# Performance work log

Measured on AMD Instinct MI355X. Metric: run time of the kernel, lower is better.

## Reference

```python
import jax, jax.numpy as jnp
import numpy as np
import math

B, S, DIM, H = 2, 2048, 1024, 16
Q_DIM = 64                 # cfg.pair_dim
V_DIM = Q_DIM * 3 // 2     # 96
MAX_POS = 2048             # cfg.rope_max_position
EPS = 1e-8
SOFTCAP = 5.0


def apply_rope(x):
    # x: [B, S, H, D]; faithful to torch version: freq = 1/logspace(0, log10(max_pos), D//2)
    D = x.shape[-1]
    nf = D // 2
    freq = 1.0 / jnp.logspace(0.0, math.log10(MAX_POS), nf, dtype=x.dtype)   # [nf]
    positions = jnp.arange(x.shape[1], dtype=x.dtype)                         # [S]
    theta = positions[:, None] * freq                                         # [S, nf]
    sin_t = jnp.sin(theta)[None, :, None, :]                                  # [1,S,1,nf]
    cos_t = jnp.cos(theta)[None, :, None, :]
    x1 = x[..., ::2]
    x2 = x[..., 1::2]
    return jnp.concatenate([x1 * cos_t - x2 * sin_t, x1 * sin_t + x2 * cos_t], axis=-1)


def setup_inputs() -> dict:
    key = jax.random.key(0)
    ks = jax.random.split(key, 9)
    x = jax.random.normal(ks[0], (B, S, DIM), dtype=jnp.float32)
    attention_bias = jax.random.normal(ks[1], (B, H, S, S), dtype=jnp.float32)
    rms_weight = jnp.ones((DIM,), dtype=jnp.float32)
    sd = 1.0 / math.sqrt(DIM)
    Wq = jax.random.normal(ks[2], (DIM, H * Q_DIM), dtype=jnp.float32) * sd
    Wk = jax.random.normal(ks[3], (DIM, Q_DIM), dtype=jnp.float32) * sd
    Wv = jax.random.normal(ks[4], (DIM, V_DIM), dtype=jnp.float32) * sd
    bv = jax.random.normal(ks[5], (V_DIM,), dtype=jnp.float32) * sd
    Wo = jax.random.normal(ks[6], (H * V_DIM, DIM), dtype=jnp.float32) / math.sqrt(H * V_DIM)
    bo = jax.random.normal(ks[7], (DIM,), dtype=jnp.float32) * sd
    return {"x": x, "attention_bias": attention_bias, "rms_weight": rms_weight,
            "Wq": Wq, "Wk": Wk, "Wv": Wv, "bv": bv, "Wo": Wo, "bo": bo}


def reference(x, attention_bias, rms_weight, Wq, Wk, Wv, bv, Wo, bo):
    # RMSNorm
    xn = x * rms_weight / jnp.sqrt(jnp.mean(x * x, axis=-1, keepdims=True) + EPS)
    # projections (MQA: single shared k and v head)
    q = (xn @ Wq).reshape(B, S, H, Q_DIM)          # [B,S,H,Dq]
    k = xn @ Wk                                     # [B,S,Dq]
    v = xn @ Wv + bv                                # [B,S,Dv]
    # RoPE
    q = apply_rope(q)
    k = apply_rope(k[:, :, None, :])[:, :, 0, :]
    # attention logits with tanh soft-cap and external bias: [B,H,S,S]
    logits = jnp.einsum('bihd,bjd->bhij', q, k)
    logits = jnp.tanh((logits + attention_bias) / SOFTCAP) * SOFTCAP
    attn = jax.nn.softmax(logits, axis=-1)
    # context: shared V across heads
    ctx = jnp.einsum('bhij,bjd->bihd', attn, v).reshape(B, S, H * V_DIM)
    return ctx @ Wo + bo
```

## Files before the change

kernel.cpp:

```cpp
#include <hip/hip_runtime.h>
#include <math.h>

#define B_   2
#define S_   2048
#define DIM_ 1024
#define H_   16
#define QD_  64
#define VD_  96
#define NQKV 1184
#define EPS_ 1e-8f

using half_t = _Float16;
using half8  = __attribute__((ext_vector_type(8))) _Float16;
using half4v = __attribute__((ext_vector_type(4))) _Float16;
using f32x4  = __attribute__((ext_vector_type(4))) float;

__global__ __launch_bounds__(256) void rmsnorm_h(const float* __restrict__ x,
                                                 const float* __restrict__ w,
                                                 half_t* __restrict__ xn) {
    int row = blockIdx.x;
    int t = threadIdx.x;
    float4 v = ((const float4*)(x + (size_t)row * DIM_))[t];
    float ss = v.x * v.x + v.y * v.y + v.z * v.z + v.w * v.w;
#pragma unroll
    for (int off = 32; off > 0; off >>= 1) ss += __shfl_down(ss, off, 64);
    __shared__ float wsum[4];
    if ((t & 63) == 0) wsum[t >> 6] = ss;
    __syncthreads();
    float tot = wsum[0] + wsum[1] + wsum[2] + wsum[3];
    float scale = rsqrtf(tot * (1.0f / DIM_) + EPS_);
    float4 wv = ((const float4*)w)[t];
    half4v o;
    o[0] = (half_t)(v.x * wv.x * scale);
    o[1] = (half_t)(v.y * wv.y * scale);
    o[2] = (half_t)(v.z * wv.z * scale);
    o[3] = (half_t)(v.w * wv.w * scale);
    ((half4v*)(xn + (size_t)row * DIM_))[t] = o;
}

template <typename TIN>
__global__ __launch_bounds__(256) void transpose_cvt(const TIN* __restrict__ in,
                                                     half_t* __restrict__ out,
                                                     int R, int C, int ldin,
                                                     size_t zin, size_t zout) {
    __shared__ float tile[32][33];
    in += (size_t)blockIdx.z * zin;
    out += (size_t)blockIdx.z * zout;
    int tx = threadIdx.x & 31, ty = threadIdx.x >> 5;
#pragma unroll
    for (int i = 0; i < 32; i += 8) {
        int r = blockIdx.y * 32 + ty + i, c = blockIdx.x * 32 + tx;
        tile[ty + i][tx] = (float)in[(size_t)r * ldin + c];
    }
    __syncthreads();
#pragma unroll
    for (int i = 0; i < 32; i += 8) {
        int orow = blockIdx.x * 32 + ty + i, ocol = blockIdx.y * 32 + tx;
        out[(size_t)orow * R + ocol] = (half_t)tile[tx][ty + i];
    }
}

__global__ __launch_bounds__(256) void fill_qkv_bias(const float* __restrict__ bv,
                                                     float* __restrict__ bq) {
    int i = blockIdx.x * 256 + threadIdx.x;
    if (i < NQKV) bq[i] = (i >= H_ * QD_ + QD_) ? bv[i - (H_ * QD_ + QD_)] : 0.0f;
}

template <typename OutT, bool BIAS>
__global__ __launch_bounds__(256) void gemm_h(const half_t* __restrict__ A,
                                              const half_t* __restrict__ BT,
                                              OutT* __restrict__ C,
                                              const float* __restrict__ bias,
                                              int M, int N, int K) {
    __shared__ half_t As[64][40];
    __shared__ half_t Bs[128][40];
    int t = threadIdx.x;
    int w = t >> 6, lane = t & 63, l15 = lane & 15, l4 = lane >> 4;
    int wm = (w >> 1) * 32, wn = (w & 1) * 64;
    int m0 = blockIdx.y * 64, n0 = blockIdx.x * 128;
    int r0 = t >> 2, off0 = (t & 3) * 8;
    f32x4 acc[2][4] = {};
    const half8 hz = {};

    const half_t* Ap = A + (size_t)(m0 + r0) * K + off0;
    const half_t* Bp0 = BT + (size_t)(n0 + r0) * K + off0;
    const half_t* Bp1 = Bp0 + (size_t)64 * K;
    bool bok0 = (n0 + r0) < N, bok1 = (n0 + r0 + 64) < N;

    half8 a0 = *(const half8*)Ap;
    half8 b0 = bok0 ? *(const half8*)Bp0 : hz;
    half8 b1 = bok1 ? *(const half8*)Bp1 : hz;

    for (int k0 = 0; k0 < K; k0 += 32) {
        __syncthreads();
        *(half8*)&As[r0][off0] = a0;
        *(half8*)&Bs[r0][off0] = b0;
        *(half8*)&Bs[r0 + 64][off0] = b1;
        __syncthreads();
        if (k0 + 32 < K) {
            a0 = *(const half8*)(Ap + k0 + 32);
            b0 = bok0 ? *(const half8*)(Bp0 + k0 + 32) : hz;
            b1 = bok1 ? *(const half8*)(Bp1 + k0 + 32) : hz;
        }
        half8 af[2], bf[4];
#pragma unroll
        for (int mt = 0; mt < 2; ++mt) af[mt] = *(const half8*)&As[wm + mt * 16 + l15][l4 * 8];
#pragma unroll
        for (int nt = 0; nt < 4; ++nt) bf[nt] = *(const half8*)&Bs[wn + nt * 16 + l15][l4 * 8];
#pragma unroll
        for (int mt = 0; mt < 2; ++mt)
#pragma unroll
            for (int nt = 0; nt < 4; ++nt)
                acc[mt][nt] =
                    __builtin_amdgcn_mfma_f32_16x16x32_f16(af[mt], bf[nt], acc[mt][nt], 0, 0, 0);
    }

#pragma unroll
    for (int mt = 0; mt < 2; ++mt)
#pragma unroll
        for (int nt = 0; nt < 4; ++nt) {
            int n = n0 + wn + nt * 16 + l15;
            if (n < N) {
#pragma unroll
                for (int reg = 0; reg < 4; ++reg) {
                    int m = m0 + wm + mt * 16 + l4 * 4 + reg;
                    float v = acc[mt][nt][reg];
                    if (BIAS) v += bias[n];
                    C[(size_t)m * N + n] = (OutT)v;
                }
            }
        }
}

__global__ __launch_bounds__(256) void rope_h(const half_t* __restrict__ in, int ldin,
                                              half_t* __restrict__ out,
                                              int hc, int total_pairs) {
    int p = blockIdx.x * 256 + threadIdx.x;
    if (p >= total_pairs) return;
    int i = p & 31;
    int chunk = p >> 5;
    int row = chunk / hc;
    int h = chunk - row * hc;
    int s = row & (S_ - 1);
    const half_t* src = in + (size_t)row * ldin + h * 64 + 2 * i;
    float x1 = (float)src[0], x2 = (float)src[1];
    float freq = exp2f((float)i * (-11.0f / 31.0f));
    float th = (float)s * freq;
    float sn, cs;
    sincosf(th, &sn, &cs);
    half_t* dst = out + (size_t)chunk * 64;
    dst[i] = (half_t)(x1 * cs - x2 * sn);
    dst[i + 32] = (half_t)(x1 * sn + x2 * cs);
}

#define C1_ 0.57707801635558534f
#define C2_ 14.426950408889634f

__global__ __launch_bounds__(256, 4) void attn_mfma(const half_t* __restrict__ qh,
                                                    const half_t* __restrict__ kh,
                                                    const half_t* __restrict__ vt,
                                                    const float* __restrict__ bias,
                                                    half_t* __restrict__ ctx) {
    __shared__ half_t ks[64][72];
    __shared__ half_t vs[96][72];
    __shared__ half_t ps[4][16][72];

    int t = threadIdx.x;
    int w = t >> 6, lane = t & 63, l15 = lane & 15, l4 = lane >> 4;
    int i0 = blockIdx.x * 64, h = blockIdx.y, b = blockIdx.z;

    const half_t* qbase =
        qh + (((size_t)(b * S_ + i0 + w * 16 + l15) * H_ + h) << 6) + l4 * 8;
    half8 qf0 = *(const half8*)qbase;
    half8 qf1 = *(const half8*)(qbase + 32);

    f32x4 cacc[6] = {};
    float rsum = 0.f;

    int sr = t >> 3, so = (t & 7) * 8;
    const float* bbase =
        bias + ((size_t)(b * H_ + h) * S_ + i0 + w * 16 + l15) * S_ + l4 * 4;
    const half_t* krow0 = kh + (((size_t)b * S_ + sr) << 6) + so;
    const half_t* krow1 = krow0 + ((size_t)32 << 6);
    const half_t* vrow0 = vt + ((size_t)b * 96 + sr) * S_ + so;
    const half_t* vrow1 = vrow0 + (size_t)32 * S_;
    const half_t* vrow2 = vrow0 + (size_t)64 * S_;

    half8 kr0, kr1, vr0, vr1, vr2;
    f32x4 bc[4], bn[4];

    kr0 = *(const half8*)krow0;
    kr1 = *(const half8*)krow1;
    vr0 = *(const half8*)vrow0;
    vr1 = *(const half8*)vrow1;
    vr2 = *(const half8*)vrow2;
#pragma unroll
    for (int nt = 0; nt < 4; ++nt) {
        f32x4 bb = __builtin_nontemporal_load((const f32x4*)(bbase + nt * 16));
#pragma unroll
        for (int e = 0; e < 4; ++e) bc[nt][e] = bb[e] * C1_;
    }

    *(half8*)&ks[sr][so] = kr0;
    *(half8*)&ks[sr + 32][so] = kr1;
    *(half8*)&vs[sr][so] = vr0;
    *(half8*)&vs[sr + 32][so] = vr1;
    *(half8*)&vs[sr + 64][so] = vr2;
    __syncthreads();

    for (int j0 = 0; j0 < S_; j0 += 64) {
        int jn = j0 + 64;
        bool more = jn < S_;

        if (more) {
            kr0 = *(const half8*)(krow0 + ((size_t)jn << 6));
            kr1 = *(const half8*)(krow1 + ((size_t)jn << 6));
            vr0 = *(const half8*)(vrow0 + jn);
            vr1 = *(const half8*)(vrow1 + jn);
            vr2 = *(const half8*)(vrow2 + jn);
#pragma unroll
            for (int nt = 0; nt < 4; ++nt)
                bn[nt] = __builtin_nontemporal_load((const f32x4*)(bbase + jn + nt * 16));
        }

#pragma unroll
        for (int nt = 0; nt < 4; ++nt) {
            f32x4 s = {};
            half8 kb0 = *(const half8*)&ks[nt * 16 + l15][l4 * 8];
            half8 kb1 = *(const half8*)&ks[nt * 16 + l15][32 + l4 * 8];
            __builtin_amdgcn_s_setprio(1);
            s = __builtin_amdgcn_mfma_f32_16x16x32_f16(kb0, qf0, s, 0, 0, 0);
            s = __builtin_amdgcn_mfma_f32_16x16x32_f16(kb1, qf1, s, 0, 0, 0);
            __builtin_amdgcn_s_setprio(0);
            half4v ph;
#pragma unroll
            for (int reg = 0; reg < 4; ++reg) {
                float u = __builtin_amdgcn_exp2f(fmaf(C1_, s[reg], bc[nt][reg]));
                float p = __builtin_amdgcn_exp2f(-C2_ * __builtin_amdgcn_rcpf(u + 1.0f));
                rsum += p;
                ph[reg] = (half_t)p;
            }
            *(half4v*)&ps[w][l15][nt * 16 + l4 * 4] = ph;
        }

        __builtin_amdgcn_s_setprio(1);
#pragma unroll
        for (int hf = 0; hf < 2; ++hf) {
            half8 af = *(const half8*)&ps[w][l15][hf * 32 + l4 * 8];
#pragma unroll
            for (int nt = 0; nt < 6; ++nt) {
                half8 vv = *(const half8*)&vs[nt * 16 + l15][hf * 32 + l4 * 8];
                cacc[nt] = __builtin_amdgcn_mfma_f32_16x16x32_f16(af, vv, cacc[nt], 0, 0, 0);
            }
        }
        __builtin_amdgcn_s_setprio(0);

        if (more) {
            __syncthreads();
            *(half8*)&ks[sr][so] = kr0;
            *(half8*)&ks[sr + 32][so] = kr1;
            *(half8*)&vs[sr][so] = vr0;
            *(half8*)&vs[sr + 32][so] = vr1;
            *(half8*)&vs[sr + 64][so] = vr2;
            __syncthreads();
#pragma unroll
            for (int nt = 0; nt < 4; ++nt)
#pragma unroll
                for (int e = 0; e < 4; ++e) bc[nt][e] = bn[nt][e] * C1_;
        }
    }

    rsum += __shfl_xor(rsum, 16, 64);
    rsum += __shfl_xor(rsum, 32, 64);
    float rinv = __builtin_amdgcn_rcpf(rsum);
    float rr[4];
#pragma unroll
    for (int reg = 0; reg < 4; ++reg) rr[reg] = __shfl(rinv, l4 * 4 + reg, 64);

#pragma unroll
    for (int nt = 0; nt < 6; ++nt)
#pragma unroll
        for (int reg = 0; reg < 4; ++reg) {
            int i = i0 + w * 16 + l4 * 4 + reg;
            ctx[((size_t)(b * S_ + i) * H_ + h) * VD_ + nt * 16 + l15] =
                (half_t)(cacc[nt][reg] * rr[reg]);
        }
}

extern "C" void kernel_launch(void* const* d_in, const int* in_sizes, int n_in,
                              void* d_out, int out_size, void* d_ws, size_t ws_size,
                              hipStream_t stream) {
    (void)in_sizes; (void)n_in; (void)out_size; (void)ws_size;
    const float* x  = (const float*)d_in[0];
    const float* ab = (const float*)d_in[1];
    const float* rw = (const float*)d_in[2];
    const float* Wq = (const float*)d_in[3];
    const float* Wk = (const float*)d_in[4];
    const float* Wv = (const float*)d_in[5];
    const float* bv = (const float*)d_in[6];
    const float* Wo = (const float*)d_in[7];
    const float* bo = (const float*)d_in[8];
    float* out = (float*)d_out;

    const size_t R = (size_t)B_ * S_;
    half_t* p = (half_t*)d_ws;
    half_t* xn_h  = p;  p += R * DIM_;
    half_t* qkv_h = p;  p += R * NQKV;
    half_t* q_h   = p;  p += R * DIM_;
    half_t* k_h   = p;  p += R * QD_;
    half_t* vtb   = p;  p += R * VD_;
    half_t* ctx_h = p;  p += R * H_ * VD_;
    half_t* WqkvT = p;  p += (size_t)NQKV * DIM_;
    half_t* WoT   = p;  p += (size_t)(H_ * VD_) * DIM_;
    float*  bqkv  = (float*)p;  p += 2 * NQKV;

    rmsnorm_h<<<dim3(R), 256, 0, stream>>>(x, rw, xn_h);

    half_t* WqT = WqkvT;
    half_t* WkT = WqkvT + (size_t)(H_ * QD_) * DIM_;
    half_t* WvT = WkT + (size_t)QD_ * DIM_;
    transpose_cvt<float><<<dim3(32, 32, 1), 256, 0, stream>>>(Wq, WqT, DIM_, H_ * QD_,
                                                              H_ * QD_, 0, 0);
    transpose_cvt<float><<<dim3(2, 32, 1), 256, 0, stream>>>(Wk, WkT, DIM_, QD_, QD_, 0, 0);
    transpose_cvt<float><<<dim3(3, 32, 1), 256, 0, stream>>>(Wv, WvT, DIM_, VD_, VD_, 0, 0);
    transpose_cvt<float><<<dim3(32, 48, 1), 256, 0, stream>>>(Wo, WoT, H_ * VD_, DIM_,
                                                              DIM_, 0, 0);
    fill_qkv_bias<<<dim3((NQKV + 255) / 256), 256, 0, stream>>>(bv, bqkv);

    gemm_h<half_t, true><<<dim3(10, 64), 256, 0, stream>>>(xn_h, WqkvT, qkv_h, bqkv,
                                                           (int)R, NQKV, DIM_);

    rope_h<<<dim3((R * H_ * 32) / 256), 256, 0, stream>>>(qkv_h, NQKV, q_h, H_,
                                                          (int)(R * H_ * 32));
    rope_h<<<dim3((R * 32) / 256), 256, 0, stream>>>(qkv_h + H_ * QD_, NQKV, k_h, 1,
                                                     (int)(R * 32));

    transpose_cvt<half_t><<<dim3(3, 64, 2), 256, 0, stream>>>(
        qkv_h + H_ * QD_ + QD_, vtb, S_, VD_, NQKV, (size_t)S_ * NQKV, (size_t)VD_ * S_);

    attn_mfma<<<dim3(S_ / 64, H_, B_), 256, 0, stream>>>(q_h, k_h, vtb, ab, ctx_h);

    gemm_h<float, true><<<dim3(8, 64), 256, 0, stream>>>(ctx_h, WoT, out, bo,
                                                         (int)R, DIM_, H_ * VD_);
}
```

Before: 831.7 us.

## Load K/V MFMA fragments directly from global memory, drop shared staging and barriers

The attention kernel no longer stages K and V tiles in shared memory with two block barriers per iteration. Each wave now loads its MFMA operand fragments for K and V straight from global memory, relying on L2/L1 caching since all waves and blocks share the same K/V. The occupancy hint drops from 4 to 3 blocks per SM to leave room for the extra fragment registers. The cost is 4x redundant global/L1 traffic for K/V across waves and exposed load latency, since the loads are no longer prefetched one iteration ahead.

```diff
diff --git a/kernel.cpp b/kernel.cpp
--- a/kernel.cpp
+++ b/kernel.cpp
@@ -156,13 +156,11 @@
 #define C1_ 0.57707801635558534f
 #define C2_ 14.426950408889634f
 
-__global__ __launch_bounds__(256, 4) void attn_mfma(const half_t* __restrict__ qh,
+__global__ __launch_bounds__(256, 3) void attn_mfma(const half_t* __restrict__ qh,
                                                     const half_t* __restrict__ kh,
                                                     const half_t* __restrict__ vt,
                                                     const float* __restrict__ bias,
                                                     half_t* __restrict__ ctx) {
-    __shared__ half_t ks[64][72];
-    __shared__ half_t vs[96][72];
     __shared__ half_t ps[4][16][72];
 
     int t = threadIdx.x;
@@ -177,60 +175,47 @@
     f32x4 cacc[6] = {};
     float rsum = 0.f;
 
-    int sr = t >> 3, so = (t & 7) * 8;
     const float* bbase =
         bias + ((size_t)(b * H_ + h) * S_ + i0 + w * 16 + l15) * S_ + l4 * 4;
-    const half_t* krow0 = kh + (((size_t)b * S_ + sr) << 6) + so;
-    const half_t* krow1 = krow0 + ((size_t)32 << 6);
-    const half_t* vrow0 = vt + ((size_t)b * 96 + sr) * S_ + so;
-    const half_t* vrow1 = vrow0 + (size_t)32 * S_;
-    const half_t* vrow2 = vrow0 + (size_t)64 * S_;
-
-    half8 kr0, kr1, vr0, vr1, vr2;
+    const half_t* kfb = kh + (((size_t)b * S_ + l15) << 6) + l4 * 8;
+    const half_t* vfb = vt + ((size_t)b * 96 + l15) * S_ + l4 * 8;
+
     f32x4 bc[4], bn[4];
-
-    kr0 = *(const half8*)krow0;
-    kr1 = *(const half8*)krow1;
-    vr0 = *(const half8*)vrow0;
-    vr1 = *(const half8*)vrow1;
-    vr2 = *(const half8*)vrow2;
 #pragma unroll
     for (int nt = 0; nt < 4; ++nt) {
         f32x4 bb = __builtin_nontemporal_load((const f32x4*)(bbase + nt * 16));
 #pragma unroll
         for (int e = 0; e < 4; ++e) bc[nt][e] = bb[e] * C1_;
     }
-
-    *(half8*)&ks[sr][so] = kr0;
-    *(half8*)&ks[sr + 32][so] = kr1;
-    *(half8*)&vs[sr][so] = vr0;
-    *(half8*)&vs[sr + 32][so] = vr1;
-    *(half8*)&vs[sr + 64][so] = vr2;
-    __syncthreads();
 
     for (int j0 = 0; j0 < S_; j0 += 64) {
         int jn = j0 + 64;
         bool more = jn < S_;
 
         if (more) {
-            kr0 = *(const half8*)(krow0 + ((size_t)jn << 6));
-            kr1 = *(const half8*)(krow1 + ((size_t)jn << 6));
-            vr0 = *(const half8*)(vrow0 + jn);
-            vr1 = *(const half8*)(vrow1 + jn);
-            vr2 = *(const half8*)(vrow2 + jn);
 #pragma unroll
             for (int nt = 0; nt < 4; ++nt)
                 bn[nt] = __builtin_nontemporal_load((const f32x4*)(bbase + jn + nt * 16));
         }
 
+        half8 kb0[4], kb1[4];
+#pragma unroll
+        for (int nt = 0; nt < 4; ++nt) {
+            const half_t* kp = kfb + ((size_t)(j0 + nt * 16) << 6);
+            kb0[nt] = *(const half8*)kp;
+            kb1[nt] = *(const half8*)(kp + 32);
+        }
+        half8 vv0[6];
+#pragma unroll
+        for (int nt = 0; nt < 6; ++nt)
+            vv0[nt] = *(const half8*)(vfb + (size_t)nt * 16 * S_ + j0);
+
 #pragma unroll
         for (int nt = 0; nt < 4; ++nt) {
             f32x4 s = {};
-            half8 kb0 = *(const half8*)&ks[nt * 16 + l15][l4 * 8];
-            half8 kb1 = *(const half8*)&ks[nt * 16 + l15][32 + l4 * 8];
             __builtin_amdgcn_s_setprio(1);
-            s = __builtin_amdgcn_mfma_f32_16x16x32_f16(kb0, qf0, s, 0, 0, 0);
-            s = __builtin_amdgcn_mfma_f32_16x16x32_f16(kb1, qf1, s, 0, 0, 0);
+            s = __builtin_amdgcn_mfma_f32_16x16x32_f16(kb0[nt], qf0, s, 0, 0, 0);
+            s = __builtin_amdgcn_mfma_f32_16x16x32_f16(kb1[nt], qf1, s, 0, 0, 0);
             __builtin_amdgcn_s_setprio(0);
             half4v ph;
 #pragma unroll
@@ -243,26 +228,23 @@
             *(half4v*)&ps[w][l15][nt * 16 + l4 * 4] = ph;
         }
 
+        half8 vv1[6];
+#pragma unroll
+        for (int nt = 0; nt < 6; ++nt)
+            vv1[nt] = *(const half8*)(vfb + (size_t)nt * 16 * S_ + j0 + 32);
+
+        half8 af0 = *(const half8*)&ps[w][l15][l4 * 8];
+        half8 af1 = *(const half8*)&ps[w][l15][32 + l4 * 8];
         __builtin_amdgcn_s_setprio(1);
 #pragma unroll
-        for (int hf = 0; hf < 2; ++hf) {
-            half8 af = *(const half8*)&ps[w][l15][hf * 32 + l4 * 8];
-#pragma unroll
-            for (int nt = 0; nt < 6; ++nt) {
-                half8 vv = *(const half8*)&vs[nt * 16 + l15][hf * 32 + l4 * 8];
-                cacc[nt] = __builtin_amdgcn_mfma_f32_16x16x32_f16(af, vv, cacc[nt], 0, 0, 0);
-            }
-        }
+        for (int nt = 0; nt < 6; ++nt)
+            cacc[nt] = __builtin_amdgcn_mfma_f32_16x16x32_f16(af0, vv0[nt], cacc[nt], 0, 0, 0);
+#pragma unroll
+        for (int nt = 0; nt < 6; ++nt)
+            cacc[nt] = __builtin_amdgcn_mfma_f32_16x16x32_f16(af1, vv1[nt], cacc[nt], 0, 0, 0);
         __builtin_amdgcn_s_setprio(0);
 
         if (more) {
-            __syncthreads();
-            *(half8*)&ks[sr][so] = kr0;
-            *(half8*)&ks[sr + 32][so] = kr1;
-            *(half8*)&vs[sr][so] = vr0;
-            *(half8*)&vs[sr + 32][so] = vr1;
-            *(half8*)&vs[sr + 64][so] = vr2;
-            __syncthreads();
 #pragma unroll
             for (int nt = 0; nt < 4; ++nt)
 #pragma unroll
```

Result: slower. 1.028 ms (+23.6%).
